# Kernel optimization log

Hardware: AMD Instinct MI355X
Metric: run time of the kernel (lower is better)

Reference implementation:

```python
import jax, jax.numpy as jnp
import numpy as np

B, N, T = 512, 128, 64
ALPHA = 0.5  # LeakyReLU negative slope
NEG = jnp.float32(-9e15)


def _gat(h, mask, W, a):
    # GraphAttentionLayer with concat=True (trailing relu), eval mode (no dropout)
    Wh = h @ W                                   # [B,N,F]
    F = W.shape[1]
    e1 = Wh @ a[:F]                              # [B,N,1]
    e2 = Wh @ a[F:]                              # [B,N,1]
    e = jax.nn.leaky_relu(e1 + jnp.swapaxes(e2, 1, 2), ALPHA)  # [B,N,N]
    e = jnp.where(mask, e, NEG)
    att = jax.nn.softmax(e, axis=1)              # torch softmax dim=1 (over rows)
    return jax.nn.relu(jnp.matmul(att, Wh))


def _lstm_layer(x, wih, whh, bih, bhh):
    # x: [T,B,in]; hidden size 1; torch gate order i,f,g,o
    h0 = jnp.zeros((x.shape[1], 1), x.dtype)
    def step(carry, xt):
        h, c = carry
        g = xt @ wih.T + h @ whh.T + bih + bhh   # [B,4]
        i, f, gg, o = jnp.split(g, 4, axis=-1)
        c = jax.nn.sigmoid(f) * c + jax.nn.sigmoid(i) * jnp.tanh(gg)
        h = jax.nn.sigmoid(o) * jnp.tanh(c)
        return (h, c), h
    _, ys = jax.lax.scan(step, (h0, h0), x)
    return ys                                    # [T,B,1]


def setup_inputs() -> dict:
    key = jax.random.key(0)
    ks = jax.random.split(key, 32)
    def xu(k, shape, gain=1.414):
        lim = gain * np.sqrt(6.0 / (shape[0] + shape[1]))
        return jax.random.uniform(k, shape, jnp.float32, -lim, lim)
    d = {}
    d["adjacency"] = jax.random.randint(ks[0], (B, N, N), 0, 2, dtype=jnp.int32)
    d["feature"] = jax.random.normal(ks[1], (B, N), jnp.float32)
    d["time"] = jax.random.normal(ks[2], (B, N), jnp.float32)
    d["interval_popularity"] = jax.random.normal(ks[3], (B, T), jnp.float32)
    # GAT params
    d["W1"] = xu(ks[4], (1, 512)); d["a1"] = xu(ks[5], (1024, 1))
    d["W2"] = xu(ks[6], (512, 8)); d["a2"] = xu(ks[7], (16, 1))
    # attention-pooling params (torch.randn in original)
    d["Weight"] = jax.random.normal(ks[8], (128, 128), jnp.float32)
    d["Wv"] = jax.random.normal(ks[9], (128, 128), jnp.float32)
    # 2-layer LSTM(1->1)
    d["wih0"] = jax.random.normal(ks[10], (4, 1)) * 0.5
    d["whh0"] = jax.random.normal(ks[11], (4, 1)) * 0.5
    d["bih0"] = jax.random.normal(ks[12], (4,)) * 0.5
    d["bhh0"] = jax.random.normal(ks[13], (4,)) * 0.5
    d["wih1"] = jax.random.normal(ks[14], (4, 1)) * 0.5
    d["whh1"] = jax.random.normal(ks[15], (4, 1)) * 0.5
    d["bih1"] = jax.random.normal(ks[16], (4,)) * 0.5
    d["bhh1"] = jax.random.normal(ks[17], (4,)) * 0.5
    # MultiheadAttention(embed_dim=1, heads=1)
    d["mha_in_w"] = jax.random.normal(ks[18], (3, 1)) * 0.5
    d["mha_in_b"] = jnp.zeros((3,), jnp.float32)
    d["mha_out_w"] = jax.random.normal(ks[19], (1, 1)) * 0.5
    d["mha_out_b"] = jnp.zeros((1,), jnp.float32)
    # FL MLP: 192->128->32->1 (stored as [in,out])
    d["fl1_w"] = xu(ks[20], (192, 128), 1.0); d["fl1_b"] = jnp.zeros((128,), jnp.float32)
    d["fl2_w"] = xu(ks[21], (128, 32), 1.0);  d["fl2_b"] = jnp.zeros((32,), jnp.float32)
    d["fl3_w"] = xu(ks[22], (32, 1), 1.0);    d["fl3_b"] = jnp.zeros((1,), jnp.float32)
    return d


def reference(adjacency, feature, time, interval_popularity,
              W1, a1, W2, a2, Weight, Wv,
              wih0, whh0, bih0, bhh0, wih1, whh1, bih1, bhh1,
              mha_in_w, mha_in_b, mha_out_w, mha_out_b,
              fl1_w, fl1_b, fl2_w, fl2_b, fl3_w, fl3_b):
    mask = adjacency > 0
    x = feature.reshape(B, N, -1)                # [B,128,1]
    h = _gat(x, mask, W1, a1)                    # [B,128,512]
    h = jax.nn.relu(h)
    h = _gat(h, mask, W2, a2)                    # [B,128,8]

    xs = jnp.swapaxes(interval_popularity.reshape(B, -1, 1), 0, 1)  # [T,B,1]
    xs = _lstm_layer(xs, wih0, whh0, bih0, bhh0)
    xs = _lstm_layer(xs, wih1, whh1, bih1, bhh1)
    ip = jnp.swapaxes(xs, 0, 1).reshape(B, -1)   # [B,64]

    h = jnp.mean(h, axis=2, keepdims=True)       # [B,128,1]
    Wt = time.reshape(B, N, -1)                  # [B,128,1]
    att = jnp.concatenate([h, Wt], axis=2)       # [B,128,2]
    att = jnp.swapaxes(jnp.swapaxes(att, 1, 2) @ Weight, 1, 2)  # [B,128,2]
    att = jax.nn.softmax(att, axis=2)
    hv = jnp.swapaxes(jnp.concatenate([h, Wt], axis=2), 1, 2)   # [B,2,128]
    hv = jax.nn.relu((hv @ Wv).reshape(B, N, -1))  # faithful reshape (not transpose)
    h = jnp.sum(hv * att, axis=2)                # [B,128]

    h = jnp.concatenate([h, ip], axis=1)         # [B,192]
    hq = h[..., None]                            # [B,192,1]
    q = hq * mha_in_w[0, 0] + mha_in_b[0]
    k = hq * mha_in_w[1, 0] + mha_in_b[1]
    v = hq * mha_in_w[2, 0] + mha_in_b[2]
    a = jax.nn.softmax(q @ jnp.swapaxes(k, 1, 2), axis=-1)  # scale=1/sqrt(1)
    ho = (a @ v) * mha_out_w[0, 0] + mha_out_b[0]
    h = (ho + hq).reshape(B, -1)                 # [B,192]

    h = jax.nn.relu(h @ fl1_w + fl1_b)
    h = jnp.tanh(h @ fl2_w + fl2_b)
    h = jax.nn.relu(h @ fl3_w + fl3_b)           # [B,1]
    return h
```

## Files before the change

### kernel.cpp

```cpp
#include <hip/hip_runtime.h>
#include <math.h>

typedef unsigned int uint;
typedef unsigned long long ull;

#define L2E 1.44269504f

__device__ __forceinline__ float lrelu(float z){ return fmaxf(z, 0.5f*z); }
__device__ __forceinline__ float reluf(float z){ return fmaxf(z, 0.f); }
__device__ __forceinline__ float fexp(float z){ return __builtin_amdgcn_exp2f(z*L2E); }
__device__ __forceinline__ float frcp(float z){ return __builtin_amdgcn_rcpf(z); }
__device__ __forceinline__ float tanh_n(float z){
  return __fmaf_rn(2.f, __builtin_amdgcn_rcpf(1.f + __builtin_amdgcn_exp2f(-2.f*L2E*z)), -1.f);
}

__global__ __launch_bounds__(512) void fused_kernel(
    const int* __restrict__ adj, const float* __restrict__ feat,
    const float* __restrict__ timei,
    const float* __restrict__ Weight, const float* __restrict__ Wv,
    const float* __restrict__ W1, const float* __restrict__ a1,
    const float* __restrict__ W2, const float* __restrict__ a2,
    const float* __restrict__ ipop,
    const float* __restrict__ wih0, const float* __restrict__ whh0,
    const float* __restrict__ bih0, const float* __restrict__ bhh0,
    const float* __restrict__ wih1, const float* __restrict__ whh1,
    const float* __restrict__ bih1, const float* __restrict__ bhh1,
    const float* __restrict__ mha_in_w, const float* __restrict__ mha_in_b,
    const float* __restrict__ mha_out_w, const float* __restrict__ mha_out_b,
    const float* __restrict__ fl1_w, const float* __restrict__ fl1_b,
    const float* __restrict__ fl2_w, const float* __restrict__ fl2_b,
    const float* __restrict__ fl3_w, const float* __restrict__ fl3_b,
    float* __restrict__ out)
{
  const int b = blockIdx.x, t = threadIdx.x;
  const int lane = t & 127, h = t >> 7;
  const int wv = t >> 6, ln = t & 63;

  __shared__ ull   rowW[256];
  __shared__ float xs[128], tim[128], hm[128], eAs[128], thr1[128];
  __shared__ float2 f2a[128];
  __shared__ float2 red4[4][128];
  __shared__ float4 q4[128];
  __shared__ float4 pool4[4][128];
  __shared__ float2 kv[192];
  __shared__ float  hq[192], h2s[192];
  __shared__ float  pden[2][192], pnum[2][192];
  __shared__ float  sred[8];
  __shared__ float  cpart[8][2];
  __shared__ float  pqpart[8][16];
  __shared__ float  cons[24];
  __shared__ float  ips[64];

  if (t < 128){ xs[t] = feat[b*128 + t]; tim[t] = timei[b*128 + t]; }

  float a2reg[16];
  if (t == 0){
    #pragma unroll
    for (int g = 0; g < 16; ++g) a2reg[g] = a2[g];
  }

  float h1v=0.f, c1s=0.f, h2v=0.f, c2s=0.f;
  float wi0s[4], wh0s[4], bb0s[4], wi1s[4], wh1s[4], bb1s[4];
  const float4* xsrc4 = (const float4*)(ipop + b*64);
  float4 xcur0, xcur1;
  if (t == 511){
    #pragma unroll
    for (int k = 0; k < 4; ++k){
      const float s = (k == 2) ? -2.f*L2E : -L2E;
      wi0s[k]=wih0[k]*s; wh0s[k]=whh0[k]*s; bb0s[k]=(bih0[k]+bhh0[k])*s;
      wi1s[k]=wih1[k]*s; wh1s[k]=whh1[k]*s; bb1s[k]=(bih1[k]+bhh1[k])*s;
    }
    xcur0 = xsrc4[0]; xcur1 = xsrc4[1];
  }
  auto lstm8 = [&](int c){
    if (t != 511) return;
    const float4 xa = xcur0, xb = xcur1;
    if (c < 7){ xcur0 = xsrc4[2*c+2]; xcur1 = xsrc4[2*c+3]; }
    float o[8];
    #pragma unroll
    for (int si = 0; si < 8; ++si){
      const float x = (si==0)?xa.x:(si==1)?xa.y:(si==2)?xa.z:(si==3)?xa.w:
                      (si==4)?xb.x:(si==5)?xb.y:(si==6)?xb.z:xb.w;
      float gi = frcp(1.f + __builtin_amdgcn_exp2f(__fmaf_rn(x, wi0s[0], __fmaf_rn(h1v, wh0s[0], bb0s[0]))));
      float gf = frcp(1.f + __builtin_amdgcn_exp2f(__fmaf_rn(x, wi0s[1], __fmaf_rn(h1v, wh0s[1], bb0s[1]))));
      float gg = __fmaf_rn(2.f, frcp(1.f + __builtin_amdgcn_exp2f(__fmaf_rn(x, wi0s[2], __fmaf_rn(h1v, wh0s[2], bb0s[2])))), -1.f);
      float go = frcp(1.f + __builtin_amdgcn_exp2f(__fmaf_rn(x, wi0s[3], __fmaf_rn(h1v, wh0s[3], bb0s[3]))));
      c1s = gf*c1s + gi*gg;  h1v = go*tanh_n(c1s);
      float hi = frcp(1.f + __builtin_amdgcn_exp2f(__fmaf_rn(h1v, wi1s[0], __fmaf_rn(h2v, wh1s[0], bb1s[0]))));
      float hf = frcp(1.f + __builtin_amdgcn_exp2f(__fmaf_rn(h1v, wi1s[1], __fmaf_rn(h2v, wh1s[1], bb1s[1]))));
      float hg = __fmaf_rn(2.f, frcp(1.f + __builtin_amdgcn_exp2f(__fmaf_rn(h1v, wi1s[2], __fmaf_rn(h2v, wh1s[2], bb1s[2])))), -1.f);
      float ho = frcp(1.f + __builtin_amdgcn_exp2f(__fmaf_rn(h1v, wi1s[3], __fmaf_rn(h2v, wh1s[3], bb1s[3])))) ;
      c2s = hf*c2s + hi*hg;  h2v = ho*tanh_n(c2s);
      o[si] = h2v;
    }
    #pragma unroll
    for (int si = 0; si < 8; ++si) ips[8*c + si] = o[si];
  };

  {
    const int* abase = adj + (((long)b) << 14) + wv*2048 + ln;
    ull myword = 0;
    #pragma unroll
    for (int blk = 0; blk < 4; ++blk){
      int v[8];
      #pragma unroll
      for (int q = 0; q < 8; ++q) v[q] = abase[(blk*8 + q)*64];
      #pragma unroll
      for (int q = 0; q < 8; ++q){
        ull m = __ballot(v[q] > 0);
        myword = (ln == blk*8 + q) ? m : myword;
      }
    }
    if (ln < 32) rowW[wv*32 + ln] = myword;
  }

  {
    float w0 = W1[t];
    float s1 = w0*a1[t];
    float s2 = w0*a1[512+t];
    #pragma unroll
    for (int off = 32; off; off >>= 1){ s1 += __shfl_xor(s1, off); s2 += __shfl_xor(s2, off); }
    if (ln == 0){ cpart[wv][0] = s1; cpart[wv][1] = s2; }
  }
  {
    const float w = W1[t];
    const float wp = fmaxf(w, 0.f), wn = fminf(w, 0.f);
    const float4 A = *(const float4*)(W2 + t*8);
    const float4 Bv = *(const float4*)(W2 + t*8 + 4);
    float accP[8], accQ[8];
    accP[0]=wp*A.x;  accQ[0]=wn*A.x;   accP[1]=wp*A.y;  accQ[1]=wn*A.y;
    accP[2]=wp*A.z;  accQ[2]=wn*A.z;   accP[3]=wp*A.w;  accQ[3]=wn*A.w;
    accP[4]=wp*Bv.x; accQ[4]=wn*Bv.x;  accP[5]=wp*Bv.y; accQ[5]=wn*Bv.y;
    accP[6]=wp*Bv.z; accQ[6]=wn*Bv.z;  accP[7]=wp*Bv.w; accQ[7]=wn*Bv.w;
    #pragma unroll
    for (int g = 0; g < 8; ++g){
      float p = accP[g], q = accQ[g];
      #pragma unroll
      for (int off = 32; off; off >>= 1){ p += __shfl_xor(p, off); q += __shfl_xor(q, off); }
      if (ln == 0){ pqpart[wv][g] = p; pqpart[wv][8+g] = q; }
    }
  }
  __syncthreads();

  const uint rowm = (uint)(rowW[lane*2 + (h>>1)] >> ((h&1)*32));
  uint colm = 0;
  {
    const int wsel = lane >> 6, bsel = lane & 63;
    #pragma unroll 8
    for (int k = 0; k < 32; ++k)
      colm |= (uint)((rowW[(32*h + k)*2 + wsel] >> bsel) & 1ull) << k;
  }
  if (t < 64){
    float mx = fmaxf(xs[t], xs[t+64]);
    float mn = fminf(xs[t], xs[t+64]);
    #pragma unroll
    for (int off = 32; off; off >>= 1){
      mx = fmaxf(mx, __shfl_xor(mx, off));
      mn = fminf(mn, __shfl_xor(mn, off));
    }
    if (t == 0){ sred[0] = mx; sred[1] = mn; }
  }
  if (t == 0){
    float c1v = 0.f, c2v = 0.f;
    #pragma unroll
    for (int wvi = 0; wvi < 8; ++wvi){ c1v += cpart[wvi][0]; c2v += cpart[wvi][1]; }
    cons[0] = c1v; cons[1] = c2v;
    float pAx=0.f, qAx=0.f, pBx=0.f, qBx=0.f;
    #pragma unroll
    for (int g = 0; g < 8; ++g){
      float P = 0.f, Q = 0.f;
      #pragma unroll
      for (int wvi = 0; wvi < 8; ++wvi){ P += pqpart[wvi][g]; Q += pqpart[wvi][8+g]; }
      cons[2+g] = P; cons[10+g] = Q;
      pAx = __fmaf_rn(P, a2reg[g],   pAx);  qAx = __fmaf_rn(Q, a2reg[g],   qAx);
      pBx = __fmaf_rn(P, a2reg[8+g], pBx);  qBx = __fmaf_rn(Q, a2reg[8+g], qBx);
    }
    cons[18]=pAx; cons[19]=qAx; cons[20]=pBx; cons[21]=qBx;
  }
  lstm8(0);
  __syncthreads();

  float myE1=0.f, myEh=0.f, myA=0.f, myB=0.f, mythr=0.f, myx=0.f;
  {
    const float c1 = cons[0], c2 = cons[1];
    const float rmax = (c1 >= 0.f) ? c1*sred[0] : c1*sred[1];
    if (t < 128){
      myx = xs[t];
      float r  = c1*myx;
      float cj = c2*myx;
      float cb = lrelu(rmax + cj);
      myE1  = fexp(r - rmax);
      myEh  = fexp(0.5f*(r - rmax));
      myA   = fexp(rmax + cj - cb);
      myB   = fexp(0.5f*(rmax + cj) - cb);
      mythr = fexp(-cj - rmax);
      f2a[t] = make_float2(myE1, myEh);
      thr1[t] = mythr;
    }
  }
  lstm8(1);
  __syncthreads();

  {
    const float thrj = thr1[lane];
    float s1 = 0.f, s2 = 0.f;
    #pragma unroll 8
    for (int k = 0; k < 32; ++k){
      float2 E = f2a[32*h + k];
      bool m = ((colm >> k) & 1u);
      bool cond = (E.x >= thrj);
      s1 += (m &&  cond) ? E.x : 0.f;
      s2 += (m && !cond) ? E.y : 0.f;
    }
    red4[h][lane] = make_float2(s1, s2);
  }
  lstm8(2);
  __syncthreads();

  if (t < 128){
    float sx = 0.f, sy = 0.f;
    #pragma unroll
    for (int g = 0; g < 4; ++g){ float2 v = red4[g][t]; sx += v.x; sy += v.y; }
    float den = __fmaf_rn(myA, sx, myB*sy);
    float cr = frcp(den);
    q4[t] = make_float4(myA*cr*myx, myB*cr*myx, mythr, 0.f);
  }
  lstm8(3);
  __syncthreads();

  {
    const float2 Eo = f2a[lane];
    float t1 = 0.f, t2 = 0.f;
    #pragma unroll 8
    for (int k = 0; k < 32; ++k){
      float4 G = q4[32*h + k];
      bool m = ((rowm >> k) & 1u);
      bool cond = (Eo.x >= G.z);
      t1 += (m &&  cond) ? G.x : 0.f;
      t2 += (m && !cond) ? G.y : 0.f;
    }
    red4[h][lane] = make_float2(t1, t2);
  }
  lstm8(4);
  __syncthreads();

  float u = 0.f, eBv = 0.f, eAv = 0.f;
  if (t < 128){
    float sx = 0.f, sy = 0.f;
    #pragma unroll
    for (int g = 0; g < 4; ++g){ float2 v = red4[g][t]; sx += v.x; sy += v.y; }
    u = __fmaf_rn(myE1, sx, myEh*sy);
    eAv = (u >= 0.f ? cons[18] : cons[19])*u;
    eBv = (u >= 0.f ? cons[20] : cons[21])*u;
    eAs[t] = eAv;
  }
  lstm8(5);
  __syncthreads();

  if (t < 64){
    float mx = fmaxf(eAs[t], eAs[t+64]);
    #pragma unroll
    for (int off = 32; off; off >>= 1) mx = fmaxf(mx, __shfl_xor(mx, off));
    if (t == 0) sred[2] = mx;
  }
  lstm8(6);
  __syncthreads();

  float myE1b=0.f, myEhb=0.f, myA2=0.f, myB2=0.f;
  {
    const float eAmax = sred[2];
    if (t < 128){
      float cb = lrelu(eAmax + eBv);
      myE1b = fexp(eAv - eAmax);
      myEhb = fexp(0.5f*(eAv - eAmax));
      myA2  = fexp(eAmax + eBv - cb);
      myB2  = fexp(0.5f*(eAmax + eBv) - cb);
      float th = fexp(-eBv - eAmax);
      f2a[t] = make_float2(myE1b, myEhb);
      thr1[t] = th;
    }
  }
  lstm8(7);
  __syncthreads();

  {
    const float thrj = thr1[lane];
    float s1 = 0.f, s2 = 0.f;
    #pragma unroll 8
    for (int k = 0; k < 32; ++k){
      float2 E = f2a[32*h + k];
      bool m = ((colm >> k) & 1u);
      bool cond = (E.x >= thrj);
      s1 += (m &&  cond) ? E.x : 0.f;
      s2 += (m && !cond) ? E.y : 0.f;
    }
    red4[h][lane] = make_float2(s1, s2);
  }
  __syncthreads();

  if (t < 128){
    float sx = 0.f, sy = 0.f;
    #pragma unroll
    for (int g = 0; g < 4; ++g){ float2 v = red4[g][t]; sx += v.x; sy += v.y; }
    float den = __fmaf_rn(myA2, sx, myB2*sy);
    float cr = frcp(den);
    float up = fmaxf(u, 0.f), un = fminf(u, 0.f);
    q4[t] = make_float4(myA2*cr*up, myB2*cr*up, myA2*cr*un, myB2*cr*un);
  }
  __syncthreads();

  {
    const float2 Eo = f2a[lane];
    float sp1=0.f, sp2=0.f, sn1=0.f, sn2=0.f;
    #pragma unroll 8
    for (int k = 0; k < 32; ++k){
      int j = 32*h + k;
      float4 G = q4[j];
      float thj = thr1[j];
      bool m = ((rowm >> k) & 1u);
      bool cond = (Eo.x >= thj);
      sp1 += (m &&  cond) ? G.x : 0.f;
      sp2 += (m && !cond) ? G.y : 0.f;
      sn1 += (m &&  cond) ? G.z : 0.f;
      sn2 += (m && !cond) ? G.w : 0.f;
    }
    pool4[h][lane] = make_float4(sp1, sp2, sn1, sn2);
  }
  __syncthreads();

  if (t < 128){
    float sx=0.f, sy=0.f, sz=0.f, sw=0.f;
    #pragma unroll
    for (int g = 0; g < 4; ++g){ float4 v = pool4[g][t]; sx+=v.x; sy+=v.y; sz+=v.z; sw+=v.w; }
    float sp = __fmaf_rn(myE1b, sx, myEhb*sy);
    float sn = __fmaf_rn(myE1b, sz, myEhb*sw);
    float acc = 0.f;
    #pragma unroll
    for (int g = 0; g < 8; ++g) acc += reluf(__fmaf_rn(sp, cons[2+g], sn*cons[10+g]));
    hm[t] = 0.125f*acc;
  }
  __syncthreads();

  {
    const int n = lane;
    float a0=0.f, a1v=0.f, v0=0.f, v1=0.f;
    const int m0 = h*32;
    #pragma unroll 4
    for (int k = 0; k < 32; ++k){
      int m = m0 + k;
      float hmv = hm[m], tv = tim[m];
      float wg = Weight[(m<<7) + n], wvv = Wv[(m<<7) + n];
      a0 = __fmaf_rn(hmv, wg, a0); a1v = __fmaf_rn(tv, wg, a1v);
      v0 = __fmaf_rn(hmv, wvv, v0); v1 = __fmaf_rn(tv, wvv, v1);
    }
    pool4[h][n] = make_float4(a0, a1v, v0, v1);
  }
  __syncthreads();

  float att0 = 0.f, att1 = 0.f, rsv = 0.f;
  if (t < 128){
    float A0=0.f, A1=0.f, V0=0.f, V1=0.f;
    #pragma unroll
    for (int g = 0; g < 4; ++g){ float4 v = pool4[g][t]; A0+=v.x; A1+=v.y; V0+=v.z; V1+=v.w; }
    red4[0][t] = make_float2(V0, V1);
    float mx = fmaxf(A0, A1);
    att0 = fexp(A0 - mx); att1 = fexp(A1 - mx);
    rsv = frcp(att0 + att1);
  }
  __syncthreads();

  if (t < 128){
    float r0, r1;
    if (t < 64){ r0 = red4[0][2*t].x;     r1 = red4[0][2*t+1].x; }
    else       { r0 = red4[0][2*t-128].y; r1 = red4[0][2*t-127].y; }
    hq[t] = (reluf(r0)*att0 + reluf(r1)*att1)*rsv;
  }
  if (t >= 192 && t < 256) hq[128 + (t - 192)] = ips[t - 192];
  __syncthreads();

  const float wq = mha_in_w[0], wk = mha_in_w[1], wvv_ = mha_in_w[2];
  const float bq = mha_in_b[0], bk = mha_in_b[1], bv = mha_in_b[2];
  const float wo = mha_out_w[0], bo = mha_out_b[0];
  if (t < 192){
    float hv_ = hq[t];
    kv[t] = make_float2(__fmaf_rn(hv_, wk, bk), __fmaf_rn(hv_, wvv_, bv));
  }
  __syncthreads();

  if (t < 64){
    float k0 = kv[t].x, k1 = kv[t+64].x, k2 = kv[t+128].x;
    float mx = fmaxf(fmaxf(k0, k1), k2);
    float mn = fminf(fminf(k0, k1), k2);
    #pragma unroll
    for (int off = 32; off; off >>= 1){
      mx = fmaxf(mx, __shfl_xor(mx, off));
      mn = fminf(mn, __shfl_xor(mn, off));
    }
    if (t == 0){ sred[3] = mx; sred[4] = mn; }
  }
  __syncthreads();

  if (t < 384){
    const int half = (t >= 192), tt = t - half*192;
    float qi = __fmaf_rn(hq[tt], wq, bq);
    float mx = (qi >= 0.f) ? qi*sred[3] : qi*sred[4];
    const float qi2 = qi*L2E, mx2 = mx*L2E;
    float den = 0.f, num = 0.f;
    const int j0 = half*96;
    #pragma unroll 8
    for (int jj = 0; jj < 96; ++jj){
      float2 K = kv[j0 + jj];
      float e = __builtin_amdgcn_exp2f(__fmaf_rn(qi2, K.x, -mx2));
      den += e; num = __fmaf_rn(e, K.y, num);
    }
    pden[half][tt] = den; pnum[half][tt] = num;
  }
  __syncthreads();

  if (t < 192){
    float den = pden[0][t] + pden[1][t];
    float num = pnum[0][t] + pnum[1][t];
    h2s[t] = __fmaf_rn(num*frcp(den), wo, bo) + hq[t];
  }
  __syncthreads();

  {
    const int n = t & 127, qtr = t >> 7;
    float acc = 0.f;
    const int i0 = qtr*48;
    #pragma unroll 8
    for (int k = 0; k < 48; ++k){
      int i = i0 + k;
      acc = __fmaf_rn(h2s[i], fl1_w[i*128 + n], acc);
    }
    red4[qtr][n].x = acc;
  }
  __syncthreads();

  if (t < 128) thr1[t] = reluf(red4[0][t].x + red4[1][t].x + red4[2][t].x + red4[3][t].x + fl1_b[t]);
  __syncthreads();

  if (t < 128){
    const int n = t & 31, seg = t >> 5;
    float p = 0.f;
    #pragma unroll 8
    for (int k = 0; k < 32; ++k){
      int i = seg*32 + k;
      p = __fmaf_rn(thr1[i], fl2_w[i*32 + n], p);
    }
    eAs[t] = p;
  }
  __syncthreads();

  if (t < 32) hm[t] = tanh_n(eAs[t] + eAs[t+32] + eAs[t+64] + eAs[t+96] + fl2_b[t]);
  __syncthreads();

  if (t < 64){
    float p = (t < 32) ? hm[t]*fl3_w[t] : 0.f;
    #pragma unroll
    for (int off = 32; off; off >>= 1) p += __shfl_xor(p, off);
    if (t == 0) out[b] = reluf(p + fl3_b[0]);
  }
}

extern "C" void kernel_launch(void* const* d_in, const int* in_sizes, int n_in,
                              void* d_out, int out_size, void* d_ws, size_t ws_size,
                              hipStream_t stream) {
  const int*   adj    = (const int*)  d_in[0];
  const float* feat   = (const float*)d_in[1];
  const float* timei  = (const float*)d_in[2];
  const float* ipop   = (const float*)d_in[3];
  const float* W1     = (const float*)d_in[4];
  const float* a1     = (const float*)d_in[5];
  const float* W2     = (const float*)d_in[6];
  const float* a2     = (const float*)d_in[7];
  const float* Weight = (const float*)d_in[8];
  const float* Wv     = (const float*)d_in[9];
  const float* wih0   = (const float*)d_in[10];
  const float* whh0   = (const float*)d_in[11];
  const float* bih0   = (const float*)d_in[12];
  const float* bhh0   = (const float*)d_in[13];
  const float* wih1   = (const float*)d_in[14];
  const float* whh1   = (const float*)d_in[15];
  const float* bih1   = (const float*)d_in[16];
  const float* bhh1   = (const float*)d_in[17];
  const float* mha_in_w  = (const float*)d_in[18];
  const float* mha_in_b  = (const float*)d_in[19];
  const float* mha_out_w = (const float*)d_in[20];
  const float* mha_out_b = (const float*)d_in[21];
  const float* fl1_w = (const float*)d_in[22];
  const float* fl1_b = (const float*)d_in[23];
  const float* fl2_w = (const float*)d_in[24];
  const float* fl2_b = (const float*)d_in[25];
  const float* fl3_w = (const float*)d_in[26];
  const float* fl3_b = (const float*)d_in[27];

  fused_kernel<<<512, 512, 0, stream>>>(adj, feat, timei, Weight, Wv,
                                        W1, a1, W2, a2, ipop,
                                        wih0, whh0, bih0, bhh0,
                                        wih1, whh1, bih1, bhh1,
                                        mha_in_w, mha_in_b, mha_out_w, mha_out_b,
                                        fl1_w, fl1_b, fl2_w, fl2_b, fl3_w, fl3_b,
                                        (float*)d_out);
}
```

Measured before the change: 43.90 us.

## Replace threshold-split leaky-ReLU softmax sums with single max-based factorized sums

```diff
diff --git a/kernel.cpp b/kernel.cpp
--- a/kernel.cpp
+++ b/kernel.cpp
@@ -37,8 +37,9 @@
   const int wv = t >> 6, ln = t & 63;
 
   __shared__ ull   rowW[256];
-  __shared__ float xs[128], tim[128], hm[128], eAs[128], thr1[128];
+  __shared__ float xs[128], tim[128], hm[128], eAs[128], rho_s[128];
   __shared__ float2 f2a[128];
+  __shared__ float  red1[4][128];
   __shared__ float2 red4[4][128];
   __shared__ float4 q4[128];
   __shared__ float4 pool4[4][128];
@@ -180,7 +181,7 @@
   lstm8(0);
   __syncthreads();
 
-  float myE1=0.f, myEh=0.f, myA=0.f, myB=0.f, mythr=0.f, myx=0.f;
+  float myE1=0.f, myRho=0.f, myx=0.f;
   {
     const float c1 = cons[0], c2 = cons[1];
     const float rmax = (c1 >= 0.f) ? c1*sred[0] : c1*sred[1];
@@ -188,68 +189,58 @@
       myx = xs[t];
       float r  = c1*myx;
       float cj = c2*myx;
-      float cb = lrelu(rmax + cj);
-      myE1  = fexp(r - rmax);
-      myEh  = fexp(0.5f*(r - rmax));
-      myA   = fexp(rmax + cj - cb);
-      myB   = fexp(0.5f*(rmax + cj) - cb);
-      mythr = fexp(-cj - rmax);
-      f2a[t] = make_float2(myE1, myEh);
-      thr1[t] = mythr;
+      float d  = r - rmax;
+      myE1 = fexp(d);
+      float Eh = fexp(0.5f*d);
+      myRho = fexp(-0.5f*fmaxf(rmax + cj, -170.f));
+      f2a[t] = make_float2(myE1, Eh);
+      rho_s[t] = myRho;
     }
   }
   lstm8(1);
   __syncthreads();
 
   {
-    const float thrj = thr1[lane];
-    float s1 = 0.f, s2 = 0.f;
+    const float rho = rho_s[lane];
+    float s = 0.f;
     #pragma unroll 8
     for (int k = 0; k < 32; ++k){
       float2 E = f2a[32*h + k];
-      bool m = ((colm >> k) & 1u);
-      bool cond = (E.x >= thrj);
-      s1 += (m &&  cond) ? E.x : 0.f;
-      s2 += (m && !cond) ? E.y : 0.f;
-    }
-    red4[h][lane] = make_float2(s1, s2);
+      float v = fmaxf(E.x, rho*E.y);
+      s += ((colm >> k) & 1u) ? v : 0.f;
+    }
+    red1[h][lane] = s;
   }
   lstm8(2);
   __syncthreads();
 
   if (t < 128){
-    float sx = 0.f, sy = 0.f;
-    #pragma unroll
-    for (int g = 0; g < 4; ++g){ float2 v = red4[g][t]; sx += v.x; sy += v.y; }
-    float den = __fmaf_rn(myA, sx, myB*sy);
-    float cr = frcp(den);
-    q4[t] = make_float4(myA*cr*myx, myB*cr*myx, mythr, 0.f);
+    float s = red1[0][t] + red1[1][t] + red1[2][t] + red1[3][t];
+    float sinv = frcp(s);
+    float ax = fabsf(myx)*sinv;
+    q4[t] = make_float4(ax, myRho*ax, (myx >= 0.f) ? 1.f : -1.f, 0.f);
   }
   lstm8(3);
   __syncthreads();
 
   {
-    const float2 Eo = f2a[lane];
-    float t1 = 0.f, t2 = 0.f;
+    const float om = frcp(f2a[lane].y);
+    float acc = 0.f;
     #pragma unroll 8
     for (int k = 0; k < 32; ++k){
       float4 G = q4[32*h + k];
-      bool m = ((rowm >> k) & 1u);
-      bool cond = (Eo.x >= G.z);
-      t1 += (m &&  cond) ? G.x : 0.f;
-      t2 += (m && !cond) ? G.y : 0.f;
-    }
-    red4[h][lane] = make_float2(t1, t2);
+      float v = fmaxf(G.x, om*G.y);
+      float sg = ((rowm >> k) & 1u) ? G.z : 0.f;
+      acc = __fmaf_rn(v, sg, acc);
+    }
+    red1[h][lane] = acc;
   }
   lstm8(4);
   __syncthreads();
 
   float u = 0.f, eBv = 0.f, eAv = 0.f;
   if (t < 128){
-    float sx = 0.f, sy = 0.f;
-    #pragma unroll
-    for (int g = 0; g < 4; ++g){ float2 v = red4[g][t]; sx += v.x; sy += v.y; }
-    u = __fmaf_rn(myE1, sx, myEh*sy);
+    u = myE1*(red1[0][t] + red1[1][t] + red1[2][t] + red1[3][t]);
     eAv = (u >= 0.f ? cons[18] : cons[19])*u;
     eBv = (u >= 0.f ? cons[20] : cons[21])*u;
     eAs[t] = eAv;
@@ -266,74 +257,64 @@
   lstm8(6);
   __syncthreads();
 
-  float myE1b=0.f, myEhb=0.f, myA2=0.f, myB2=0.f;
+  float myE1b=0.f;
   {
     const float eAmax = sred[2];
     if (t < 128){
-      float cb = lrelu(eAmax + eBv);
-      myE1b = fexp(eAv - eAmax);
-      myEhb = fexp(0.5f*(eAv - eAmax));
-      myA2  = fexp(eAmax + eBv - cb);
-      myB2  = fexp(0.5f*(eAmax + eBv) - cb);
-      float th = fexp(-eBv - eAmax);
-      f2a[t] = make_float2(myE1b, myEhb);
-      thr1[t] = th;
+      float d2 = eAv - eAmax;
+      myE1b = fexp(d2);
+      float Ehb = fexp(0.5f*d2);
+      float rho2 = fexp(-0.5f*fmaxf(eAmax + eBv, -170.f));
+      f2a[t] = make_float2(myE1b, Ehb);
+      rho_s[t] = rho2;
     }
   }
   lstm8(7);
   __syncthreads();
 
   {
-    const float thrj = thr1[lane];
-    float s1 = 0.f, s2 = 0.f;
+    const float rho = rho_s[lane];
+    float s = 0.f;
     #pragma unroll 8
     for (int k = 0; k < 32; ++k){
       float2 E = f2a[32*h + k];
-      bool m = ((colm >> k) & 1u);
-      bool cond = (E.x >= thrj);
-      s1 += (m &&  cond) ? E.x : 0.f;
-      s2 += (m && !cond) ? E.y : 0.f;
-    }
-    red4[h][lane] = make_float2(s1, s2);
-  }
-  __syncthreads();
-
-  if (t < 128){
-    float sx = 0.f, sy = 0.f;
-    #pragma unroll
-    for (int g = 0; g < 4; ++g){ float2 v = red4[g][t]; sx += v.x; sy += v.y; }
-    float den = __fmaf_rn(myA2, sx, myB2*sy);
-    float cr = frcp(den);
-    float up = fmaxf(u, 0.f), un = fminf(u, 0.f);
-    q4[t] = make_float4(myA2*cr*up, myB2*cr*up, myA2*cr*un, myB2*cr*un);
-  }
-  __syncthreads();
-
-  {
-    const float2 Eo = f2a[lane];
-    float sp1=0.f, sp2=0.f, sn1=0.f, sn2=0.f;
-    #pragma unroll 8
-    for (int k = 0; k < 32; ++k){
-      int j = 32*h + k;
-      float4 G = q4[j];
-      float thj = thr1[j];
+      float v = fmaxf(E.x, rho*E.y);
+      s += ((colm >> k) & 1u) ? v : 0.f;
+    }
+    red1[h][lane] = s;
+  }
+  __syncthreads();
+
+  if (t < 128){
+    float s = red1[0][t] + red1[1][t] + red1[2][t] + red1[3][t];
+    float sinv = frcp(s);
+    float rho2 = rho_s[t];
+    float up = fmaxf(u, 0.f)*sinv, un = -fminf(u, 0.f)*sinv;
+    q4[t] = make_float4(up, rho2*up, un, rho2*un);
+  }
+  __syncthreads();
+
+  {
+    const float om = frcp(f2a[lane].y);
+    float accp = 0.f, accn = 0.f;
+    #pragma unroll 8
+    for (int k = 0; k < 32; ++k){
+      float4 G = q4[32*h + k];
       bool m = ((rowm >> k) & 1u);
-      bool cond = (Eo.x >= thj);
-      sp1 += (m &&  cond) ? G.x : 0.f;
-      sp2 += (m && !cond) ? G.y : 0.f;
-      sn1 += (m &&  cond) ? G.z : 0.f;
-      sn2 += (m && !cond) ? G.w : 0.f;
-    }
-    pool4[h][lane] = make_float4(sp1, sp2, sn1, sn2);
-  }
-  __syncthreads();
-
-  if (t < 128){
-    float sx=0.f, sy=0.f, sz=0.f, sw=0.f;
-    #pragma unroll
-    for (int g = 0; g < 4; ++g){ float4 v = pool4[g][t]; sx+=v.x; sy+=v.y; sz+=v.z; sw+=v.w; }
-    float sp = __fmaf_rn(myE1b, sx, myEhb*sy);
-    float sn = __fmaf_rn(myE1b, sz, myEhb*sw);
+      float v1 = fmaxf(G.x, om*G.y);
+      float v2 = fmaxf(G.z, om*G.w);
+      accp += m ? v1 : 0.f;
+      accn += m ? v2 : 0.f;
+    }
+    red4[h][lane] = make_float2(accp, accn);
+  }
+  __syncthreads();
+
+  if (t < 128){
+    float ap=0.f, an=0.f;
+    #pragma unroll
+    for (int g = 0; g < 4; ++g){ float2 v = red4[g][t]; ap += v.x; an += v.y; }
+    float sp = myE1b*ap, sn = -myE1b*an;
     float acc = 0.f;
     #pragma unroll
     for (int g = 0; g < 8; ++g) acc += reluf(__fmaf_rn(sp, cons[2+g], sn*cons[10+g]));
@@ -437,7 +418,7 @@
   }
   __syncthreads();
 
-  if (t < 128) thr1[t] = reluf(red4[0][t].x + red4[1][t].x + red4[2][t].x + red4[3][t].x + fl1_b[t]);
+  if (t < 128) rho_s[t] = reluf(red4[0][t].x + red4[1][t].x + red4[2][t].x + red4[3][t].x + fl1_b[t]);
   __syncthreads();
 
   if (t < 128){
@@ -446,7 +427,7 @@
     #pragma unroll 8
     for (int k = 0; k < 32; ++k){
       int i = seg*32 + k;
-      p = __fmaf_rn(thr1[i], fl2_w[i*32 + n], p);
+      p = __fmaf_rn(rho_s[i], fl2_w[i*32 + n], p);
     }
     eAs[t] = p;
   }
```

Measured after the change: 42.83 us, median of 2. 2.4% less time.
